# Kernel tuning notes

Hardware: AMD Instinct MI355X
Metric: run time of the kernel (lower is better)

## Reference

```python
import jax, jax.numpy as jnp
import numpy as np

DIM = 1024
HEADS = 16
HEAD_DIM = DIM // HEADS
SCALE = float(HEAD_DIM ** (-0.25))
ROPE_BASE = 10000.0


def apply_rope(x):
    # x: [B, N, H, D], rotate-half RoPE over last dim
    B, N, H, D = x.shape
    half = D // 2
    inv_freq = 1.0 / (ROPE_BASE ** (jnp.arange(half, dtype=jnp.float32) / half))
    freqs = jnp.arange(N, dtype=jnp.float32)[:, None] * inv_freq[None, :]  # [N, half]
    cos = jnp.cos(freqs)[None, :, None, :].astype(x.dtype)  # [1,N,1,half]
    sin = jnp.sin(freqs)[None, :, None, :].astype(x.dtype)
    x1, x2 = x[..., :half], x[..., half:]
    return jnp.concatenate([x1 * cos - x2 * sin, x1 * sin + x2 * cos], axis=-1)


def setup_inputs() -> dict:
    key = jax.random.key(0)
    k1, k2, k3 = jax.random.split(key, 3)
    x = jax.random.normal(k1, (4, 4096, DIM), dtype=jnp.float32)
    w_qkv = jax.random.normal(k2, (DIM, 3 * DIM), dtype=jnp.float32) * 0.02
    w_out = jax.random.normal(k3, (DIM, DIM), dtype=jnp.float32) * 0.02
    return {"x": x, "w_qkv": w_qkv, "w_out": w_out}


def reference(x, w_qkv, w_out):
    B, N, D = x.shape
    qkv = x @ w_qkv  # [B, N, 3*D]
    q, k, v = jnp.split(qkv, 3, axis=-1)
    q = q.reshape(B, N, HEADS, HEAD_DIM)
    k = k.reshape(B, N, HEADS, HEAD_DIM)
    v = v.reshape(B, N, HEADS, HEAD_DIM)
    q = apply_rope(q)
    k = apply_rope(k)
    # ELU(x*scale) + 1 feature map (positive)
    q = jax.nn.elu(q * SCALE) + 1.0
    k = jax.nn.elu(k * SCALE) + 1.0

    # sequential linear-attention recurrence over tokens (lax.scan)
    qT = jnp.moveaxis(q, 1, 0)  # [N, B, H, D]
    kT = jnp.moveaxis(k, 1, 0)
    vT = jnp.moveaxis(v, 1, 0)

    kv0 = jnp.zeros((B, HEADS, HEAD_DIM, HEAD_DIM), dtype=q.dtype)
    ks0 = jnp.zeros((B, HEADS, HEAD_DIM), dtype=q.dtype)

    def step(carry, qkv_t):
        kv, ks = carry
        qt, kt, vt = qkv_t
        kv = kv + jnp.einsum('bhd,bhm->bhdm', kt, vt)
        ks = ks + kt
        denom = jnp.maximum(jnp.einsum('bhd,bhd->bh', qt, ks), 1e-6)
        out_t = jnp.einsum('bhd,bhdm->bhm', qt, kv) / denom[..., None]
        return (kv, ks), out_t

    _, outT = jax.lax.scan(step, (kv0, ks0), (qT, kT, vT))  # outT: [N, B, H, D]
    out = jnp.moveaxis(outT, 0, 1).reshape(B, N, D)
    return out @ w_out
```

## Files before the change

kernel.cpp:

```cpp
#include <hip/hip_runtime.h>
#include <math.h>

#define BATCH 4
#define SEQ   4096
#define DMODEL 1024
#define HEADS 16
#define HDIM  64
#define CHUNK 64
#define NCHUNK 64
#define NTOK  16384
#define QKVC  3072
#define SCALE_F 0.35355339059327373f
#define ROPE_K 0.4152410118609203f

typedef unsigned short u16;
typedef _Float16 f16;
typedef __attribute__((ext_vector_type(8))) f16 f16x8;
typedef __attribute__((ext_vector_type(4))) float f32x4;

__device__ __forceinline__ u16 f2h(float f) { f16 h = (f16)f; return *(u16*)&h; }
__device__ __forceinline__ float h2f(u16 u) { f16 h = *(f16*)&u; return (float)h; }
__device__ __forceinline__ void storeC(u16* p, float v) { *p = f2h(v); }
__device__ __forceinline__ void storeC(float* p, float v) { *p = v; }

__device__ __forceinline__ void gload_lds16(const u16* g, u16* l)
{
    __builtin_amdgcn_global_load_lds(
        (const __attribute__((address_space(1))) void*)g,
        (__attribute__((address_space(3))) void*)l, 16, 0, 0);
}

__global__ __launch_bounds__(256)
void convert_f32_f16(const float* __restrict__ src, u16* __restrict__ dst)
{
    long i = ((long)blockIdx.x * 256 + threadIdx.x) * 4;
    float4 v = *(const float4*)(src + i);
    ushort4 o; o.x = f2h(v.x); o.y = f2h(v.y); o.z = f2h(v.z); o.w = f2h(v.w);
    *(ushort4*)(dst + i) = o;
}

__global__ __launch_bounds__(256)
void transpose_convert(const float* __restrict__ src, int C,
                       u16* __restrict__ dst, int dld)
{
    __shared__ u16 tile[64][72];
    const int r0 = blockIdx.y * 64, c0 = blockIdx.x * 64;
    const int t = threadIdx.x;
    const int rr = t >> 4, cc4 = (t & 15) * 4;
#pragma unroll
    for (int j = 0; j < 4; ++j) {
        int r = rr + j * 16;
        float4 v = *(const float4*)(src + (long)(r0 + r) * C + c0 + cc4);
        tile[cc4 + 0][r] = f2h(v.x);
        tile[cc4 + 1][r] = f2h(v.y);
        tile[cc4 + 2][r] = f2h(v.z);
        tile[cc4 + 3][r] = f2h(v.w);
    }
    __syncthreads();
#pragma unroll
    for (int j = 0; j < 4; ++j) {
        int c = rr + j * 16;
        ushort4 o = *(ushort4*)&tile[c][cc4];
        *(ushort4*)(dst + (long)(c0 + c) * dld + r0 + cc4) = o;
    }
}

template <typename CT, bool ROPE, bool SWZ>
__global__ __launch_bounds__(512, 2)
void gemm_mfma(const u16* __restrict__ A, int lda,
               const u16* __restrict__ BT, int ldbt,
               CT* __restrict__ C, int ldc, int K)
{
    __shared__ u16 ringA[4][256 * 32];
    __shared__ u16 ringB[4][256 * 32];

    const int tid = threadIdx.x;
    const int gx = gridDim.x;
    long m0, n0;
    if (SWZ) {
        const int nwg = gx * gridDim.y;
        const int bid = blockIdx.y * gx + blockIdx.x;
        const int lid = (nwg & 7) ? bid
                                  : (bid & 7) * (nwg >> 3) + (bid >> 3);
        m0 = (long)(lid / gx) * 256;
        n0 = (long)(lid % gx) * 256;
    } else {
        m0 = (long)blockIdx.y * 256;
        n0 = (long)blockIdx.x * 256;
    }

    const int w = tid >> 6, lane = tid & 63;
    const int wm = w >> 2, wn = w & 3;
    const int fr = lane & 15, quad = lane >> 4;
    const int sw = (quad ^ ((fr >> 1) & 3)) * 8;

    const int srow = tid >> 2;
    const int scol = ((tid & 3) ^ ((tid >> 3) & 3)) * 8;
    const u16* ga = A  + (m0 + srow) * (long)lda  + scol;
    const u16* gb = BT + (n0 + srow) * (long)ldbt + scol;
    const long a128 = 128 * (long)lda, b128 = 128 * (long)ldbt;

    f32x4 acc[8][4];
#pragma unroll
    for (int i = 0; i < 8; ++i)
#pragma unroll
        for (int j = 0; j < 4; ++j)
#pragma unroll
            for (int r = 0; r < 4; ++r) acc[i][j][r] = 0.0f;

    auto STAGE_A = [&](int h) {
        u16* la = &ringA[h & 3][w * 512];
        const long ko = (long)h << 5;
        gload_lds16(ga + ko,        la);
        gload_lds16(ga + ko + a128, la + 4096);
    };
    auto STAGE_B = [&](int h) {
        u16* lb = &ringB[h & 3][w * 512];
        const long ko = (long)h << 5;
        gload_lds16(gb + ko,        lb);
        gload_lds16(gb + ko + b128, lb + 4096);
    };

    STAGE_A(0); STAGE_B(0);
    STAGE_A(1); STAGE_B(1);
    STAGE_A(2); STAGE_B(2);
    asm volatile("s_waitcnt vmcnt(8)" ::: "memory");
    __builtin_amdgcn_s_barrier();

    const int NH = K >> 5;
    for (int h = 0; h < NH; ++h) {
        const u16* As_ = ringA[h & 3];
        const u16* Bs_ = ringB[h & 3];
        f16x8 af0[4], af1[4], bf[4];

#pragma unroll
        for (int mi = 0; mi < 4; ++mi)
            af0[mi] = *(const f16x8*)&As_[(wm * 128 + mi * 16 + fr) * 32 + sw];
#pragma unroll
        for (int nj = 0; nj < 4; ++nj)
            bf[nj] = *(const f16x8*)&Bs_[(wn * 64 + nj * 16 + fr) * 32 + sw];
        if (h < NH - 3) STAGE_A(h + 3);

        __builtin_amdgcn_s_setprio(1);
#pragma unroll
        for (int mi = 0; mi < 4; ++mi)
#pragma unroll
            for (int nj = 0; nj < 4; ++nj)
                acc[mi][nj] = __builtin_amdgcn_mfma_f32_16x16x32_f16(
                    af0[mi], bf[nj], acc[mi][nj], 0, 0, 0);
        __builtin_amdgcn_s_setprio(0);

#pragma unroll
        for (int mi = 0; mi < 4; ++mi)
            af1[mi] = *(const f16x8*)&As_[(wm * 128 + (mi + 4) * 16 + fr) * 32 + sw];
        if (h < NH - 3) STAGE_B(h + 3);

        if (h <= NH - 4) {
            asm volatile("s_waitcnt vmcnt(8)" ::: "memory");
        } else if (h == NH - 3) {
            asm volatile("s_waitcnt vmcnt(4)" ::: "memory");
        } else if (h == NH - 2) {
            asm volatile("s_waitcnt vmcnt(0)" ::: "memory");
        }
        if (h < NH - 1) {
            asm volatile("s_waitcnt lgkmcnt(0)" ::: "memory");
            __builtin_amdgcn_s_barrier();
        }

        __builtin_amdgcn_s_setprio(1);
#pragma unroll
        for (int mi = 0; mi < 4; ++mi)
#pragma unroll
            for (int nj = 0; nj < 4; ++nj)
                acc[mi + 4][nj] = __builtin_amdgcn_mfma_f32_16x16x32_f16(
                    af1[mi], bf[nj], acc[mi + 4][nj], 0, 0, 0);
        __builtin_amdgcn_s_setprio(0);
    }

    const long cm = m0 + wm * 128 + quad * 4;
    const long cn = n0 + wn * 64 + fr;

    if (ROPE && cn < 2048) {
        const float invf0 = exp2f(-(float)fr * ROPE_K);
        const float invf1 = exp2f(-(float)(fr + 16) * ROPE_K);
#pragma unroll
        for (int mi = 0; mi < 8; ++mi)
#pragma unroll
            for (int r = 0; r < 4; ++r) {
                long row = cm + mi * 16 + r;
                float n = (float)(int)(row & (SEQ - 1));
                float s0, c0, s1, c1;
                __sincosf(n * invf0, &s0, &c0);
                __sincosf(n * invf1, &s1, &c1);
                float x1 = acc[mi][0][r], x2 = acc[mi][2][r];
                float x3 = acc[mi][1][r], x4 = acc[mi][3][r];
                float u1 = (x1 * c0 - x2 * s0) * SCALE_F;
                float u2 = (x1 * s0 + x2 * c0) * SCALE_F;
                float u3 = (x3 * c1 - x4 * s1) * SCALE_F;
                float u4 = (x3 * s1 + x4 * c1) * SCALE_F;
                u1 = (u1 > 0.0f) ? (u1 + 1.0f) : __expf(u1);
                u2 = (u2 > 0.0f) ? (u2 + 1.0f) : __expf(u2);
                u3 = (u3 > 0.0f) ? (u3 + 1.0f) : __expf(u3);
                u4 = (u4 > 0.0f) ? (u4 + 1.0f) : __expf(u4);
                CT* pr = C + row * ldc + cn;
                storeC(pr, u1); storeC(pr + 16, u3);
                storeC(pr + 32, u2); storeC(pr + 48, u4);
            }
    } else {
#pragma unroll
        for (int mi = 0; mi < 8; ++mi)
#pragma unroll
            for (int nj = 0; nj < 4; ++nj)
#pragma unroll
                for (int r = 0; r < 4; ++r)
                    storeC(&C[(cm + mi * 16 + r) * ldc + cn + nj * 16], acc[mi][nj][r]);
    }
}

__global__ __launch_bounds__(256)
void chunk_sums_mfma(const u16* __restrict__ qkv,
                     u16* __restrict__ S, float* __restrict__ ksum)
{
    __shared__ u16 Kt[64][72];
    __shared__ u16 Vt[64][72];

    const int blk = blockIdx.x;
    const int c = blk & 63, bh = blk >> 6;
    const int b = bh >> 4, h = bh & 15;
    const int tid = threadIdx.x;
    const long base = (long)(b * SEQ + c * CHUNK) * QKVC + h * HDIM;

#pragma unroll
    for (int j = 0; j < 4; ++j) {
        int i4 = (j * 256 + tid) * 4;
        int t = i4 >> 6, d = i4 & 63;
        const u16* src = qkv + base + (long)t * QKVC + d;
        ushort4 kk = *(const ushort4*)(src + DMODEL);
        ushort4 vv = *(const ushort4*)(src + 2 * DMODEL);
        Kt[d + 0][t] = kk.x; Kt[d + 1][t] = kk.y;
        Kt[d + 2][t] = kk.z; Kt[d + 3][t] = kk.w;
        Vt[d + 0][t] = vv.x; Vt[d + 1][t] = vv.y;
        Vt[d + 2][t] = vv.z; Vt[d + 3][t] = vv.w;
    }
    __syncthreads();

    const int w = tid >> 6, lane = tid & 63;
    const int fr = lane & 15, quad = lane >> 4;

    f16x8 af0 = *(const f16x8*)&Vt[w * 16 + fr][quad * 8];
    f16x8 af1 = *(const f16x8*)&Vt[w * 16 + fr][32 + quad * 8];
    f32x4 acc[4];
#pragma unroll
    for (int j = 0; j < 4; ++j)
#pragma unroll
        for (int r = 0; r < 4; ++r) acc[j][r] = 0.0f;
#pragma unroll
    for (int j = 0; j < 4; ++j) {
        f16x8 b0 = *(const f16x8*)&Kt[j * 16 + fr][quad * 8];
        f16x8 b1 = *(const f16x8*)&Kt[j * 16 + fr][32 + quad * 8];
        acc[j] = __builtin_amdgcn_mfma_f32_16x16x32_f16(af0, b0, acc[j], 0, 0, 0);
        acc[j] = __builtin_amdgcn_mfma_f32_16x16x32_f16(af1, b1, acc[j], 0, 0, 0);
    }
    const long sb = (long)blk * 4096;
    const int mrow = w * 16 + quad * 4;
#pragma unroll
    for (int j = 0; j < 4; ++j)
#pragma unroll
        for (int r = 0; r < 4; ++r)
            S[sb + (mrow + r) * 64 + j * 16 + fr] = f2h(acc[j][r]);

    if (tid < 64) {
        float s = 0.0f;
        for (int t = 0; t < 64; ++t) s += h2f(Kt[tid][t]);
        ksum[(long)blk * 64 + tid] = s;
    }
}

__global__ __launch_bounds__(256)
void scan_kernel(u16* __restrict__ S, float* __restrict__ ksum)
{
    const int blk = blockIdx.x;
    const int slice = blk & 15, bh = blk >> 4;
    const int p = slice * 256 + threadIdx.x;
    const long base = (long)bh * NCHUNK * 4096 + p;
    float acc = 0.0f;
    for (int c = 0; c < NCHUNK; ++c) {
        long idx = base + (long)c * 4096;
        float tmp = h2f(S[idx]);
        S[idx] = f2h(acc);
        acc += tmp;
    }
    if (slice == 0 && threadIdx.x < 64) {
        const long kb = (long)bh * NCHUNK * 64 + threadIdx.x;
        float ka = 0.0f;
        for (int c = 0; c < NCHUNK; ++c) {
            float t = ksum[kb + (long)c * 64];
            ksum[kb + (long)c * 64] = ka;
            ka += t;
        }
    }
}

__global__ __launch_bounds__(256)
void chunk_out_mfma(u16* __restrict__ qkv,
                    const u16* __restrict__ S, const float* __restrict__ ksum)
{
    __shared__ u16 Qs[64][72];
    __shared__ u16 Ks[64][72];
    __shared__ u16 Vt[64][72];
    __shared__ u16 KVt[64][72];
    __shared__ u16 Sch[64][72];
    __shared__ float kss[64];
    __shared__ float den[64];

    const int blk = blockIdx.x;
    const int c = blk & 63, bh = blk >> 6;
    const int b = bh >> 4, h = bh & 15;
    const int tid = threadIdx.x;
    const long base = (long)(b * SEQ + c * CHUNK) * QKVC + h * HDIM;

#pragma unroll
    for (int j = 0; j < 4; ++j) {
        int i4 = (j * 256 + tid) * 4;
        int t = i4 >> 6, d = i4 & 63;
        const u16* src = qkv + base + (long)t * QKVC + d;
        *(ushort4*)&Qs[t][d] = *(const ushort4*)(src);
        *(ushort4*)&Ks[t][d] = *(const ushort4*)(src + DMODEL);
        ushort4 vv = *(const ushort4*)(src + 2 * DMODEL);
        Vt[d + 0][t] = vv.x; Vt[d + 1][t] = vv.y;
        Vt[d + 2][t] = vv.z; Vt[d + 3][t] = vv.w;
        *(ushort4*)&KVt[t][d] = *(const ushort4*)(S + (long)blk * 4096 + i4);
    }
    if (tid < 64) kss[tid] = ksum[(long)blk * 64 + tid];
    __syncthreads();

    const int w = tid >> 6, lane = tid & 63;
    const int fr = lane & 15, quad = lane >> 4;
    const int trow = w * 16 + quad * 4;

    f16x8 aq0 = *(const f16x8*)&Qs[w * 16 + fr][quad * 8];
    f16x8 aq1 = *(const f16x8*)&Qs[w * 16 + fr][32 + quad * 8];
    f32x4 sc[4];
#pragma unroll
    for (int j = 0; j < 4; ++j)
#pragma unroll
        for (int r = 0; r < 4; ++r) sc[j][r] = 0.0f;
#pragma unroll
    for (int j = 0; j < 4; ++j) {
        f16x8 b0 = *(const f16x8*)&Ks[j * 16 + fr][quad * 8];
        f16x8 b1 = *(const f16x8*)&Ks[j * 16 + fr][32 + quad * 8];
        sc[j] = __builtin_amdgcn_mfma_f32_16x16x32_f16(aq0, b0, sc[j], 0, 0, 0);
        sc[j] = __builtin_amdgcn_mfma_f32_16x16x32_f16(aq1, b1, sc[j], 0, 0, 0);
    }
#pragma unroll
    for (int j = 0; j < 4; ++j)
#pragma unroll
        for (int r = 0; r < 4; ++r) {
            int t = trow + r, s = j * 16 + fr;
            Sch[t][s] = f2h(s <= t ? sc[j][r] : 0.0f);
        }
    __syncthreads();

    if (tid < 64) {
        float dn = 0.0f;
        for (int d = 0; d < 64; ++d) dn += h2f(Qs[tid][d]) * kss[d];
        for (int s = 0; s <= tid; ++s) dn += h2f(Sch[tid][s]);
        den[tid] = 1.0f / fmaxf(dn, 1e-6f);
    }
    __syncthreads();

    f16x8 as0 = *(const f16x8*)&Sch[w * 16 + fr][quad * 8];
    f16x8 as1 = *(const f16x8*)&Sch[w * 16 + fr][32 + quad * 8];
    f32x4 oc[4];
#pragma unroll
    for (int j = 0; j < 4; ++j)
#pragma unroll
        for (int r = 0; r < 4; ++r) oc[j][r] = 0.0f;
#pragma unroll
    for (int j = 0; j < 4; ++j) {
        f16x8 b0 = *(const f16x8*)&Vt[j * 16 + fr][quad * 8];
        f16x8 b1 = *(const f16x8*)&Vt[j * 16 + fr][32 + quad * 8];
        oc[j] = __builtin_amdgcn_mfma_f32_16x16x32_f16(as0, b0, oc[j], 0, 0, 0);
        oc[j] = __builtin_amdgcn_mfma_f32_16x16x32_f16(as1, b1, oc[j], 0, 0, 0);
        f16x8 k0 = *(const f16x8*)&KVt[j * 16 + fr][quad * 8];
        f16x8 k1 = *(const f16x8*)&KVt[j * 16 + fr][32 + quad * 8];
        oc[j] = __builtin_amdgcn_mfma_f32_16x16x32_f16(aq0, k0, oc[j], 0, 0, 0);
        oc[j] = __builtin_amdgcn_mfma_f32_16x16x32_f16(aq1, k1, oc[j], 0, 0, 0);
    }
#pragma unroll
    for (int j = 0; j < 4; ++j)
#pragma unroll
        for (int r = 0; r < 4; ++r) {
            int t = trow + r;
            qkv[base + (long)t * QKVC + j * 16 + fr] = f2h(oc[j][r] * den[t]);
        }
}

extern "C" void kernel_launch(void* const* d_in, const int* in_sizes, int n_in,
                              void* d_out, int out_size, void* d_ws, size_t ws_size,
                              hipStream_t stream)
{
    const float* x     = (const float*)d_in[0];
    const float* w_qkv = (const float*)d_in[1];
    const float* w_out = (const float*)d_in[2];
    float* out = (float*)d_out;

    u16* qkv = (u16*)d_ws;
    u16* xf16  = (u16*)d_out;
    u16* wqkvT = xf16 + (size_t)NTOK * DMODEL;
    u16* S     = (u16*)d_out;
    float* ksum = (float*)((char*)d_out + 33554432);
    u16* woutT = qkv + 1024;

    dim3 blk(256);
    dim3 gblk(512);

    convert_f32_f16<<<NTOK * DMODEL / 1024, blk, 0, stream>>>(x, xf16);
    transpose_convert<<<dim3(QKVC / 64, DMODEL / 64), blk, 0, stream>>>(
        w_qkv, QKVC, wqkvT, DMODEL);

    gemm_mfma<u16, true, false><<<dim3(QKVC / 256, NTOK / 256), gblk, 0, stream>>>(
        xf16, DMODEL, wqkvT, DMODEL, qkv, QKVC, DMODEL);

    chunk_sums_mfma<<<64 * NCHUNK, blk, 0, stream>>>(qkv, S, ksum);
    scan_kernel<<<64 * 16, blk, 0, stream>>>(S, ksum);
    chunk_out_mfma<<<64 * NCHUNK, blk, 0, stream>>>(qkv, S, ksum);

    transpose_convert<<<dim3(DMODEL / 64, DMODEL / 64), blk, 0, stream>>>(
        w_out, DMODEL, woutT, QKVC);
    gemm_mfma<float, false, true><<<dim3(DMODEL / 256, NTOK / 256), gblk, 0, stream>>>(
        qkv, QKVC, woutT, QKVC, out, DMODEL, DMODEL);
}
```

Measured before the change: 351.9 us.

## Restructure GEMM mainloop into 64-wide K double buffer with four-phase pipeline

```diff
diff --git a/kernel.cpp b/kernel.cpp
--- a/kernel.cpp
+++ b/kernel.cpp
@@ -30,6 +30,15 @@
         (__attribute__((address_space(3))) void*)l, 16, 0, 0);
 }
 
+#define SYNC_IN() do { \
+    __builtin_amdgcn_s_barrier(); \
+    asm volatile("s_waitcnt lgkmcnt(0)" ::: "memory"); \
+    __builtin_amdgcn_sched_barrier(0); } while (0)
+
+#define BAR2() do { \
+    __builtin_amdgcn_s_barrier(); \
+    __builtin_amdgcn_sched_barrier(0); } while (0)
+
 __global__ __launch_bounds__(256)
 void convert_f32_f16(const float* __restrict__ src, u16* __restrict__ dst)
 {
@@ -71,8 +80,8 @@
                const u16* __restrict__ BT, int ldbt,
                CT* __restrict__ C, int ldc, int K)
 {
-    __shared__ u16 ringA[4][256 * 32];
-    __shared__ u16 ringB[4][256 * 32];
+    __shared__ u16 bufA[2][256 * 64];
+    __shared__ u16 bufB[2][256 * 64];
 
     const int tid = threadIdx.x;
     const int gx = gridDim.x;
@@ -92,13 +101,12 @@
     const int w = tid >> 6, lane = tid & 63;
     const int wm = w >> 2, wn = w & 3;
     const int fr = lane & 15, quad = lane >> 4;
-    const int sw = (quad ^ ((fr >> 1) & 3)) * 8;
-
-    const int srow = tid >> 2;
-    const int scol = ((tid & 3) ^ ((tid >> 3) & 3)) * 8;
-    const u16* ga = A  + (m0 + srow) * (long)lda  + scol;
-    const u16* gb = BT + (n0 + srow) * (long)ldbt + scol;
-    const long a128 = 128 * (long)lda, b128 = 128 * (long)ldbt;
+    const int f7 = fr & 7;
+
+    const int lr = lane >> 3;
+    const int lsl = (lane & 7) ^ lr;
+    const u16* gA = A  + (m0 + w * 16 + lr) * (long)lda  + lsl * 8;
+    const u16* gB = BT + (n0 + w * 16 + lr) * (long)ldbt + lsl * 8;
 
     f32x4 acc[8][4];
 #pragma unroll
@@ -108,73 +116,125 @@
 #pragma unroll
             for (int r = 0; r < 4; ++r) acc[i][j][r] = 0.0f;
 
-    auto STAGE_A = [&](int h) {
-        u16* la = &ringA[h & 3][w * 512];
-        const long ko = (long)h << 5;
-        gload_lds16(ga + ko,        la);
-        gload_lds16(ga + ko + a128, la + 4096);
+    auto STAGE = [&](int g) {
+        const int tau = g >> 2, u = g & 3;
+        const int b = tau & 1, hf = u & 1;
+        const long kt = (long)tau << 6;
+        if (u < 2) {
+            const u16* s = gA + (long)hf * 128 * lda + kt;
+            u16* d = &bufA[b][(hf * 128 + w * 16) * 64];
+            gload_lds16(s, d);
+            gload_lds16(s + 8 * (long)lda, d + 512);
+        } else {
+            const u16* s = gB + (long)hf * 128 * ldbt + kt;
+            u16* d = &bufB[b][(hf * 128 + w * 16) * 64];
+            gload_lds16(s, d);
+            gload_lds16(s + 8 * (long)ldbt, d + 512);
+        }
     };
-    auto STAGE_B = [&](int h) {
-        u16* lb = &ringB[h & 3][w * 512];
-        const long ko = (long)h << 5;
-        gload_lds16(gb + ko,        lb);
-        gload_lds16(gb + ko + b128, lb + 4096);
+    auto RD_A = [&](int b, int mi, int kk) -> f16x8 {
+        return *(const f16x8*)&bufA[b][(wm * 128 + mi * 16 + fr) * 64
+                                       + (((quad + kk * 4) ^ f7) << 3)];
     };
-
-    STAGE_A(0); STAGE_B(0);
-    STAGE_A(1); STAGE_B(1);
-    STAGE_A(2); STAGE_B(2);
-    asm volatile("s_waitcnt vmcnt(8)" ::: "memory");
+    auto RD_B = [&](int b, int nj, int kk) -> f16x8 {
+        return *(const f16x8*)&bufB[b][(wn * 64 + nj * 16 + fr) * 64
+                                       + (((quad + kk * 4) ^ f7) << 3)];
+    };
+
+    const int NT = K >> 6;
+    const int GMAX = 4 * NT;
+
+    for (int g = 0; g < 5; ++g) STAGE(g);
+    asm volatile("s_waitcnt vmcnt(2)" ::: "memory");
     __builtin_amdgcn_s_barrier();
-
-    const int NH = K >> 5;
-    for (int h = 0; h < NH; ++h) {
-        const u16* As_ = ringA[h & 3];
-        const u16* Bs_ = ringB[h & 3];
-        f16x8 af0[4], af1[4], bf[4];
-
+    __builtin_amdgcn_sched_barrier(0);
+
+    f16x8 af[4][2], bf[4][2];
+    for (int t = 0; t < NT; ++t) {
+        const int b = t & 1;
+        const int gb = 5 + 4 * t;
+
+#pragma unroll
+        for (int mi = 0; mi < 4; ++mi) {
+            af[mi][0] = RD_A(b, mi, 0); af[mi][1] = RD_A(b, mi, 1);
+        }
+#pragma unroll
+        for (int nj = 0; nj < 2; ++nj) {
+            bf[nj][0] = RD_B(b, nj, 0); bf[nj][1] = RD_B(b, nj, 1);
+        }
+        if (gb < GMAX) STAGE(gb);
+        SYNC_IN();
+        __builtin_amdgcn_s_setprio(1);
 #pragma unroll
         for (int mi = 0; mi < 4; ++mi)
-            af0[mi] = *(const f16x8*)&As_[(wm * 128 + mi * 16 + fr) * 32 + sw];
-#pragma unroll
-        for (int nj = 0; nj < 4; ++nj)
-            bf[nj] = *(const f16x8*)&Bs_[(wn * 64 + nj * 16 + fr) * 32 + sw];
-        if (h < NH - 3) STAGE_A(h + 3);
-
+#pragma unroll
+            for (int nj = 0; nj < 2; ++nj) {
+                acc[mi][nj] = __builtin_amdgcn_mfma_f32_16x16x32_f16(
+                    af[mi][0], bf[nj][0], acc[mi][nj], 0, 0, 0);
+                acc[mi][nj] = __builtin_amdgcn_mfma_f32_16x16x32_f16(
+                    af[mi][1], bf[nj][1], acc[mi][nj], 0, 0, 0);
+            }
+        __builtin_amdgcn_s_setprio(0);
+        BAR2();
+
+#pragma unroll
+        for (int nj = 2; nj < 4; ++nj) {
+            bf[nj][0] = RD_B(b, nj, 0); bf[nj][1] = RD_B(b, nj, 1);
+        }
+        if (gb + 1 < GMAX) STAGE(gb + 1);
+        SYNC_IN();
         __builtin_amdgcn_s_setprio(1);
 #pragma unroll
         for (int mi = 0; mi < 4; ++mi)
 #pragma unroll
-            for (int nj = 0; nj < 4; ++nj)
+            for (int nj = 2; nj < 4; ++nj) {
                 acc[mi][nj] = __builtin_amdgcn_mfma_f32_16x16x32_f16(
-                    af0[mi], bf[nj], acc[mi][nj], 0, 0, 0);
+                    af[mi][0], bf[nj][0], acc[mi][nj], 0, 0, 0);
+                acc[mi][nj] = __builtin_amdgcn_mfma_f32_16x16x32_f16(
+                    af[mi][1], bf[nj][1], acc[mi][nj], 0, 0, 0);
+            }
         __builtin_amdgcn_s_setprio(0);
-
+        BAR2();
+
+#pragma unroll
+        for (int mi = 0; mi < 4; ++mi) {
+            af[mi][0] = RD_A(b, mi + 4, 0); af[mi][1] = RD_A(b, mi + 4, 1);
+        }
+        if (gb + 2 < GMAX) STAGE(gb + 2);
+        SYNC_IN();
+        __builtin_amdgcn_s_setprio(1);
 #pragma unroll
         for (int mi = 0; mi < 4; ++mi)
-            af1[mi] = *(const f16x8*)&As_[(wm * 128 + (mi + 4) * 16 + fr) * 32 + sw];
-        if (h < NH - 3) STAGE_B(h + 3);
-
-        if (h <= NH - 4) {
-            asm volatile("s_waitcnt vmcnt(8)" ::: "memory");
-        } else if (h == NH - 3) {
-            asm volatile("s_waitcnt vmcnt(4)" ::: "memory");
-        } else if (h == NH - 2) {
+#pragma unroll
+            for (int nj = 2; nj < 4; ++nj) {
+                acc[mi + 4][nj] = __builtin_amdgcn_mfma_f32_16x16x32_f16(
+                    af[mi][0], bf[nj][0], acc[mi + 4][nj], 0, 0, 0);
+                acc[mi + 4][nj] = __builtin_amdgcn_mfma_f32_16x16x32_f16(
+                    af[mi][1], bf[nj][1], acc[mi + 4][nj], 0, 0, 0);
+            }
+        __builtin_amdgcn_s_setprio(0);
+        BAR2();
+
+        if (gb + 3 < GMAX) STAGE(gb + 3);
+        __builtin_amdgcn_s_barrier();
+        __builtin_amdgcn_sched_barrier(0);
+        __builtin_amdgcn_s_setprio(1);
+#pragma unroll
+        for (int mi = 0; mi < 4; ++mi)
+#pragma unroll
+            for (int nj = 0; nj < 2; ++nj) {
+                acc[mi + 4][nj] = __builtin_amdgcn_mfma_f32_16x16x32_f16(
+                    af[mi][0], bf[nj][0], acc[mi + 4][nj], 0, 0, 0);
+                acc[mi + 4][nj] = __builtin_amdgcn_mfma_f32_16x16x32_f16(
+                    af[mi][1], bf[nj][1], acc[mi + 4][nj], 0, 0, 0);
+            }
+        __builtin_amdgcn_s_setprio(0);
+        if (t < NT - 2) {
+            asm volatile("s_waitcnt vmcnt(2)" ::: "memory");
+        } else if (t == NT - 2) {
             asm volatile("s_waitcnt vmcnt(0)" ::: "memory");
         }
-        if (h < NH - 1) {
-            asm volatile("s_waitcnt lgkmcnt(0)" ::: "memory");
-            __builtin_amdgcn_s_barrier();
-        }
-
-        __builtin_amdgcn_s_setprio(1);
-#pragma unroll
-        for (int mi = 0; mi < 4; ++mi)
-#pragma unroll
-            for (int nj = 0; nj < 4; ++nj)
-                acc[mi + 4][nj] = __builtin_amdgcn_mfma_f32_16x16x32_f16(
-                    af1[mi], bf[nj], acc[mi + 4][nj], 0, 0, 0);
-        __builtin_amdgcn_s_setprio(0);
+        BAR2();
     }
 
     const long cm = m0 + wm * 128 + quad * 4;
```

After: 347.6 us. Within noise of the previous version (-1.2%).

## Load GEMM B fragments directly from global into double-buffered registers

Applied to the files above, without the earlier changes.

```diff
diff --git a/kernel.cpp b/kernel.cpp
--- a/kernel.cpp
+++ b/kernel.cpp
@@ -72,7 +72,6 @@
                CT* __restrict__ C, int ldc, int K)
 {
     __shared__ u16 ringA[4][256 * 32];
-    __shared__ u16 ringB[4][256 * 32];
 
     const int tid = threadIdx.x;
     const int gx = gridDim.x;
@@ -96,9 +95,10 @@
 
     const int srow = tid >> 2;
     const int scol = ((tid & 3) ^ ((tid >> 3) & 3)) * 8;
-    const u16* ga = A  + (m0 + srow) * (long)lda  + scol;
-    const u16* gb = BT + (n0 + srow) * (long)ldbt + scol;
-    const long a128 = 128 * (long)lda, b128 = 128 * (long)ldbt;
+    const u16* ga = A + (m0 + srow) * (long)lda + scol;
+    const long a128 = 128 * (long)lda;
+
+    const u16* gB = BT + (n0 + wn * 64 + fr) * (long)ldbt + quad * 8;
 
     f32x4 acc[8][4];
 #pragma unroll
@@ -114,32 +114,32 @@
         gload_lds16(ga + ko,        la);
         gload_lds16(ga + ko + a128, la + 4096);
     };
-    auto STAGE_B = [&](int h) {
-        u16* lb = &ringB[h & 3][w * 512];
-        const long ko = (long)h << 5;
-        gload_lds16(gb + ko,        lb);
-        gload_lds16(gb + ko + b128, lb + 4096);
-    };
-
-    STAGE_A(0); STAGE_B(0);
-    STAGE_A(1); STAGE_B(1);
-    STAGE_A(2); STAGE_B(2);
-    asm volatile("s_waitcnt vmcnt(8)" ::: "memory");
+
+    f16x8 bfc[4], bfn[4];
+
+#pragma unroll
+    for (int nj = 0; nj < 4; ++nj)
+        bfc[nj] = *(const f16x8*)(gB + (long)nj * 16 * ldbt);
+    STAGE_A(0); STAGE_A(1); STAGE_A(2);
+    asm volatile("s_waitcnt vmcnt(4)" ::: "memory");
     __builtin_amdgcn_s_barrier();
+    __builtin_amdgcn_sched_barrier(0);
 
     const int NH = K >> 5;
     for (int h = 0; h < NH; ++h) {
         const u16* As_ = ringA[h & 3];
-        const u16* Bs_ = ringB[h & 3];
-        f16x8 af0[4], af1[4], bf[4];
+        f16x8 af0[4], af1[4];
 
 #pragma unroll
         for (int mi = 0; mi < 4; ++mi)
             af0[mi] = *(const f16x8*)&As_[(wm * 128 + mi * 16 + fr) * 32 + sw];
-#pragma unroll
-        for (int nj = 0; nj < 4; ++nj)
-            bf[nj] = *(const f16x8*)&Bs_[(wn * 64 + nj * 16 + fr) * 32 + sw];
-        if (h < NH - 3) STAGE_A(h + 3);
+        if (h + 1 < NH) {
+            const long kb = (long)(h + 1) << 5;
+#pragma unroll
+            for (int nj = 0; nj < 4; ++nj)
+                bfn[nj] = *(const f16x8*)(gB + (long)nj * 16 * ldbt + kb);
+        }
+        if (h + 3 < NH) STAGE_A(h + 3);
 
         __builtin_amdgcn_s_setprio(1);
 #pragma unroll
@@ -147,19 +147,16 @@
 #pragma unroll
             for (int nj = 0; nj < 4; ++nj)
                 acc[mi][nj] = __builtin_amdgcn_mfma_f32_16x16x32_f16(
-                    af0[mi], bf[nj], acc[mi][nj], 0, 0, 0);
+                    af0[mi], bfc[nj], acc[mi][nj], 0, 0, 0);
         __builtin_amdgcn_s_setprio(0);
 
 #pragma unroll
         for (int mi = 0; mi < 4; ++mi)
             af1[mi] = *(const f16x8*)&As_[(wm * 128 + (mi + 4) * 16 + fr) * 32 + sw];
-        if (h < NH - 3) STAGE_B(h + 3);
 
         if (h <= NH - 4) {
-            asm volatile("s_waitcnt vmcnt(8)" ::: "memory");
-        } else if (h == NH - 3) {
-            asm volatile("s_waitcnt vmcnt(4)" ::: "memory");
-        } else if (h == NH - 2) {
+            asm volatile("s_waitcnt vmcnt(2)" ::: "memory");
+        } else if (h < NH - 1) {
             asm volatile("s_waitcnt vmcnt(0)" ::: "memory");
         }
         if (h < NH - 1) {
@@ -173,8 +170,11 @@
 #pragma unroll
             for (int nj = 0; nj < 4; ++nj)
                 acc[mi + 4][nj] = __builtin_amdgcn_mfma_f32_16x16x32_f16(
-                    af1[mi], bf[nj], acc[mi + 4][nj], 0, 0, 0);
+                    af1[mi], bfc[nj], acc[mi + 4][nj], 0, 0, 0);
         __builtin_amdgcn_s_setprio(0);
+
+#pragma unroll
+        for (int nj = 0; nj < 4; ++nj) bfc[nj] = bfn[nj];
     }
 
     const long cm = m0 + wm * 128 + quad * 4;
```

After: 428.7 us. 1.22x slower.
